# Kernel optimization log

Measured on AMD Instinct MI355X. Metric: run time of the kernel, lower is better.

## Reference

```python
import jax, jax.numpy as jnp
import numpy as np

N, F, D, C, K, E, M = 50000, 512, 128, 128, 3, 20000, 8  # nodes, feat, emb, conv, cheb K, hyperedges, edge size
EPS = 1e-5


def setup_inputs() -> dict:
    key = jax.random.key(0)
    ks = jax.random.split(key, 9)
    pos_set = jax.random.normal(ks[0], (N, F), jnp.float32)
    # each hyperedge = M distinct nodes (contiguous window => distinct, like the original expansion assumes)
    base = jax.random.randint(ks[1], (E, 1), 0, N - M)
    members = (base + jnp.arange(M, dtype=jnp.int32)[None, :]).astype(jnp.int32)  # [E, M]
    # expansion(): full directed clique (no self loops) on the E*M duplicated entries
    row, col = np.where(~np.eye(M, dtype=bool))            # M*(M-1) intra-edge pairs
    offs = np.arange(E, dtype=np.int64)[:, None] * M
    edge_index = jnp.asarray(np.stack([(offs + row[None, :]).ravel(),
                                       (offs + col[None, :]).ravel()]), jnp.int32)  # [2, E*M*(M-1)]
    batch = jnp.asarray(np.repeat(np.arange(E, dtype=np.int64), M), jnp.int32)      # [E*M]
    W_enc = jax.random.normal(ks[2], (F, D), jnp.float32) / np.float32(np.sqrt(F))
    b_enc = jnp.zeros((D,), jnp.float32)
    gn_gamma = 1.0 + 0.1 * jax.random.normal(ks[3], (D,), jnp.float32)
    gn_beta = 0.01 * jax.random.normal(ks[4], (D,), jnp.float32)
    gn_alpha = 1.0 + 0.1 * jax.random.normal(ks[5], (D,), jnp.float32)
    cheb_W = jax.random.normal(ks[6], (K, D, C), jnp.float32) / np.float32(np.sqrt(D * K))
    cheb_b = jnp.zeros((C,), jnp.float32)
    lin_W = jax.random.normal(ks[7], (2 * C, 1), jnp.float32) / np.float32(np.sqrt(2 * C))
    lin_b = jnp.zeros((1,), jnp.float32)
    return dict(pos_set=pos_set, W_enc=W_enc, b_enc=b_enc, gn_gamma=gn_gamma, gn_beta=gn_beta,
                gn_alpha=gn_alpha, cheb_W=cheb_W, cheb_b=cheb_b, lin_W=lin_W, lin_b=lin_b,
                members=members, edge_index=edge_index, batch=batch)


def reference(pos_set, W_enc, b_enc, gn_gamma, gn_beta, gn_alpha, cheb_W, cheb_b,
              lin_W, lin_b, members, edge_index, batch):
    num_entries = E * M
    # running_type == 'structure': Hardtanh(Linear(feature))
    x = jnp.clip(pos_set @ W_enc + b_enc, -1.0, 1.0)                    # [N, D]
    # partition(): duplicate node features per (node, hyperedge) incidence
    xe = x[members.reshape(-1)]                                         # [E*M, D]
    # GraphNorm (per-hyperedge group): out = gamma*(x - alpha*mean)/sqrt(var+eps) + beta
    cnt = jax.ops.segment_sum(jnp.ones((num_entries,), xe.dtype), batch, num_segments=E)  # [E]
    mean = jax.ops.segment_sum(xe, batch, num_segments=E) / cnt[:, None]
    ctr = xe - gn_alpha * mean[batch]
    var = jax.ops.segment_sum(ctr * ctr, batch, num_segments=E) / cnt[:, None]
    xe = gn_gamma * ctr / jnp.sqrt(var + EPS)[batch] + gn_beta
    # AlphaDropout is identity at eval time
    # ChebConv: sym norm, lambda_max=2 => L_hat = -D^{-1/2} A D^{-1/2} (zero diagonal)
    src, dst = edge_index[0], edge_index[1]
    deg = jax.ops.segment_sum(jnp.ones_like(src, dtype=xe.dtype), dst, num_segments=num_entries)
    w = -jax.lax.rsqrt(deg[src] * deg[dst])                             # [nE] scaled-Laplacian weights

    def Lhat(h):  # sparse matvec via gather + segment scatter-add
        return jax.ops.segment_sum(w[:, None] * h[src], dst, num_segments=num_entries)

    Tx0 = xe
    Tx1 = Lhat(Tx0)
    out = Tx0 @ cheb_W[0] + Tx1 @ cheb_W[1]
    Tkm1, Tkm2 = Tx1, Tx0
    for k in range(2, K):  # K is a small static constant
        Tk = 2.0 * Lhat(Tkm1) - Tkm2
        out = out + Tk @ cheb_W[k]
        Tkm1, Tkm2 = Tk, Tkm1
    h = jnp.clip(out + cheb_b, -1.0, 1.0)                               # Hardtanh
    # poolings per hyperedge
    y_max = jax.ops.segment_max(h, batch, num_segments=E)
    y_min = jax.ops.segment_min(h, batch, num_segments=E)
    y_norm = jnp.sqrt(jax.ops.segment_sum(h * h, batch, num_segments=E) / cnt[:, None])
    y = jnp.concatenate([y_max - y_min, y_norm], axis=1)                # [E, 2C]
    logits = y @ lin_W + lin_b
    return jax.nn.sigmoid(logits).squeeze(-1)                           # [E] link probabilities
```

## Files before the change

### kernel.cpp

```cpp
#include <hip/hip_runtime.h>
#include <hip/hip_bf16.h>

#define NN   50000
#define FF   512
#define DD   128
#define CC   128
#define EE   20000
#define MM   8
#define EPSV 1e-5f

typedef __attribute__((ext_vector_type(8)))  short bfrag;
typedef __attribute__((ext_vector_type(4)))  unsigned int u32x4;
typedef __attribute__((ext_vector_type(16))) float f32x16;

__device__ __forceinline__ f32x16 mfma32(u32x4 a, u32x4 b, f32x16 c) {
    return __builtin_amdgcn_mfma_f32_32x32x16_bf16(
        __builtin_bit_cast(bfrag, a), __builtin_bit_cast(bfrag, b), c, 0, 0, 0);
}

__device__ __forceinline__ unsigned short f2bf(float f) {
    unsigned u = __builtin_bit_cast(unsigned, f);
    unsigned r = u + 0x7FFFu + ((u >> 16) & 1u);
    return (unsigned short)(r >> 16);
}
__device__ __forceinline__ float bf2f(unsigned short h) {
    unsigned u = ((unsigned)h) << 16;
    return __builtin_bit_cast(float, u);
}
__device__ __forceinline__ void split1(float a, short& hi, short& lo) {
    unsigned short h = f2bf(a);
    hi = (short)h;
    lo = (short)f2bf(a - bf2f(h));
}

template <int CTRL>
__device__ __forceinline__ float dpp_addstep(float x) {
    const int xi = __builtin_bit_cast(int, x);
    const int yi = __builtin_amdgcn_update_dpp(xi, xi, CTRL, 0xF, 0xF, true);
    return x + __builtin_bit_cast(float, yi);
}
__device__ __forceinline__ float sum8(float x) {
    x = dpp_addstep<0xB1>(x);
    x = dpp_addstep<0x4E>(x);
    x = dpp_addstep<0x141>(x);
    return x;
}

__device__ __forceinline__ void pack_split8(const float* v, u32x4& hi, u32x4& lo) {
#pragma unroll
    for (int p = 0; p < 4; p++) {
        const unsigned u0 = __builtin_bit_cast(unsigned, v[2 * p]);
        const unsigned u1 = __builtin_bit_cast(unsigned, v[2 * p + 1]);
        const unsigned h0 = u0 & 0xFFFF0000u, h1 = u1 & 0xFFFF0000u;
        hi[p] = (u0 >> 16) | h1;
        const float r0 = v[2 * p]     - __builtin_bit_cast(float, h0);
        const float r1 = v[2 * p + 1] - __builtin_bit_cast(float, h1);
        unsigned lp;
        asm("v_cvt_pk_bf16_f32 %0, %1, %2" : "=v"(lp) : "v"(r0), "v"(r1));
        lo[p] = lp;
    }
}
__device__ __forceinline__ void pack8(const float* v, u32x4& w) {
#pragma unroll
    for (int p = 0; p < 4; p++) {
        unsigned lp;
        asm("v_cvt_pk_bf16_f32 %0, %1, %2" : "=v"(lp) : "v"(v[2 * p]), "v"(v[2 * p + 1]));
        w[p] = lp;
    }
}

__global__ void prep_kernel(const float* __restrict__ W_enc,
                            const float* __restrict__ cheb_W,
                            unsigned short* __restrict__ Ep_hi,
                            unsigned short* __restrict__ Ep_lo,
                            unsigned short* __restrict__ Wp_hi,
                            unsigned short* __restrict__ Wp_lo) {
    const int tid = blockIdx.x * blockDim.x + threadIdx.x;
    const int stride = gridDim.x * blockDim.x;
    for (int p = tid; p < 64 * 128; p += stride) {
        const int slot = p >> 7, n = p & 127;
        bfrag fh, fl;
#pragma unroll
        for (int j = 0; j < 8; j++) {
            const float v = W_enc[(size_t)(slot * 8 + j) * DD + n];
            short h, lo; split1(v, h, lo);
            fh[j] = h; fl[j] = lo;
        }
        *(bfrag*)&Ep_hi[(size_t)p * 8] = fh;
        *(bfrag*)&Ep_lo[(size_t)p * 8] = fl;
    }
    const float c1 = 1.0f / 7.0f;
    const float c2 = -47.0f / 49.0f;
    const float c3 = -1.0f / 7.0f;
    const float c4 = 12.0f / 49.0f;
    for (int p = tid; p < 32 * 128; p += stride) {
        const int slot = p >> 7, c = p & 127;
        bfrag fh, fl;
#pragma unroll
        for (int j = 0; j < 8; j++) {
            const int k = slot * 8 + j;
            float v;
            if (k < DD) {
                v = cheb_W[0 * DD * CC + k * CC + c]
                  + c1 * cheb_W[1 * DD * CC + k * CC + c]
                  + c2 * cheb_W[2 * DD * CC + k * CC + c];
            } else {
                const int d = k - DD;
                v = c3 * cheb_W[1 * DD * CC + d * CC + c]
                  + c4 * cheb_W[2 * DD * CC + d * CC + c];
            }
            short h, lo; split1(v, h, lo);
            fh[j] = h; fl[j] = lo;
        }
        *(bfrag*)&Wp_hi[(size_t)p * 8] = fh;
        *(bfrag*)&Wp_lo[(size_t)p * 8] = fl;
    }
}

__global__ __launch_bounds__(128, 4) void enc_kernel(
        const float* __restrict__ pos,
        const unsigned short* __restrict__ Ep_hi,
        const unsigned short* __restrict__ Ep_lo,
        const float* __restrict__ b_enc,
        float* __restrict__ x) {
    const int t = threadIdx.x;
    const int w = t >> 6, l = t & 63, l31 = l & 31, lg2 = l >> 5;

    int arow = blockIdx.x * 32 + l31;
    if (arow >= NN) arow = NN - 1;
    const float* aBase = pos + (size_t)arow * FF + lg2 * 8;

    f32x16 acc[2];
#pragma unroll
    for (int ntl = 0; ntl < 2; ntl++)
#pragma unroll
        for (int i = 0; i < 16; i++) acc[ntl][i] = 0.f;

    auto body = [&](float4 a0, float4 a1, int ks) {
        const float av[8] = {a0.x, a0.y, a0.z, a0.w, a1.x, a1.y, a1.z, a1.w};
        u32x4 ahi, alo;
        pack_split8(av, ahi, alo);
        const int slot = ks * 2 + lg2;
#pragma unroll
        for (int ntl = 0; ntl < 2; ntl++) {
            const int col = w * 64 + ntl * 32 + l31;
            const size_t boff = ((size_t)slot * 128 + col) * 8;
            const u32x4 bhi = *(const u32x4*)(Ep_hi + boff);
            const u32x4 blo = *(const u32x4*)(Ep_lo + boff);
            acc[ntl] = mfma32(ahi, bhi, acc[ntl]);
            acc[ntl] = mfma32(ahi, blo, acc[ntl]);
            acc[ntl] = mfma32(alo, bhi, acc[ntl]);
        }
    };

    float4 pa0 = *(const float4*)(aBase);
    float4 pa1 = *(const float4*)(aBase + 4);
    float4 pb0 = *(const float4*)(aBase + 16);
    float4 pb1 = *(const float4*)(aBase + 20);
    for (int ks = 0; ks < 32; ks += 2) {
        const float4 c0 = pa0, c1 = pa1;
        if (ks + 2 < 32) {
            pa0 = *(const float4*)(aBase + (ks + 2) * 16);
            pa1 = *(const float4*)(aBase + (ks + 2) * 16 + 4);
        }
        body(c0, c1, ks);
        const float4 d0 = pb0, d1 = pb1;
        if (ks + 3 < 32) {
            pb0 = *(const float4*)(aBase + (ks + 3) * 16);
            pb1 = *(const float4*)(aBase + (ks + 3) * 16 + 4);
        }
        body(d0, d1, ks + 1);
    }

    const int brow = blockIdx.x * 32;
#pragma unroll
    for (int ntl = 0; ntl < 2; ntl++) {
        const int col = w * 64 + ntl * 32 + l31;
        const float bias = b_enc[col];
#pragma unroll
        for (int r = 0; r < 16; r++) {
            const int row = brow + (r & 3) + 8 * (r >> 2) + 4 * lg2;
            if (row < NN) {
                const float v = acc[ntl][r] + bias;
                x[(size_t)row * DD + col] = fminf(1.0f, fmaxf(-1.0f, v));
            }
        }
    }
}

__global__ __launch_bounds__(256, 4) void edge_kernel(
        const float* __restrict__ x,
        const int* __restrict__ members,
        const unsigned short* __restrict__ Wp_hi,
        const unsigned short* __restrict__ Wp_lo,
        const float* __restrict__ gn_gamma,
        const float* __restrict__ gn_beta,
        const float* __restrict__ gn_alpha,
        const float* __restrict__ cheb_b,
        const float* __restrict__ lin_W,
        const float* __restrict__ lin_b,
        float* __restrict__ out) {
    const int t = threadIdx.x;
    const int w = t >> 6, l = t & 63, l31 = l & 31, lg2 = l >> 5;

    const int node = members[blockIdx.x * 128 + w * 32 + l31];
    const float* xrow = x + (size_t)node * DD + lg2 * 8;

    f32x16 acc[4];
#pragma unroll
    for (int nt = 0; nt < 4; nt++)
#pragma unroll
        for (int i = 0; i < 16; i++) acc[nt][i] = 0.f;

    auto body = [&](float4 a0, float4 a1, int ks) {
        const int koff = ks * 16 + lg2 * 8;
        const float4 al0 = *(const float4*)(gn_alpha + koff);
        const float4 al1 = *(const float4*)(gn_alpha + koff + 4);
        const float4 g0  = *(const float4*)(gn_gamma + koff);
        const float4 g1  = *(const float4*)(gn_gamma + koff + 4);
        const float4 b0  = *(const float4*)(gn_beta + koff);
        const float4 b1  = *(const float4*)(gn_beta + koff + 4);
        const float al[8] = {al0.x, al0.y, al0.z, al0.w, al1.x, al1.y, al1.z, al1.w};
        const float gm[8] = {g0.x, g0.y, g0.z, g0.w, g1.x, g1.y, g1.z, g1.w};
        const float bt[8] = {b0.x, b0.y, b0.z, b0.w, b1.x, b1.y, b1.z, b1.w};

        const float v[8] = {a0.x, a0.y, a0.z, a0.w, a1.x, a1.y, a1.z, a1.w};
        float s[8], q[8];
#pragma unroll
        for (int j = 0; j < 8; j++) { s[j] = v[j]; q[j] = v[j] * v[j]; }
#pragma unroll
        for (int j = 0; j < 8; j++) s[j] = dpp_addstep<0xB1>(s[j]);
#pragma unroll
        for (int j = 0; j < 8; j++) q[j] = dpp_addstep<0xB1>(q[j]);
#pragma unroll
        for (int j = 0; j < 8; j++) s[j] = dpp_addstep<0x4E>(s[j]);
#pragma unroll
        for (int j = 0; j < 8; j++) q[j] = dpp_addstep<0x4E>(q[j]);
#pragma unroll
        for (int j = 0; j < 8; j++) s[j] = dpp_addstep<0x141>(s[j]);
#pragma unroll
        for (int j = 0; j < 8; j++) q[j] = dpp_addstep<0x141>(q[j]);

        float nv[8], sv[8];
#pragma unroll
        for (int j = 0; j < 8; j++) {
            const float m   = s[j] * 0.125f;
            const float var = q[j] * 0.125f - al[j] * (2.0f - al[j]) * m * m;
            const float sc  = gm[j] * rsqrtf(var + EPSV);
            nv[j] = sc * (v[j] - al[j] * m) + bt[j];
            sv[j] = 8.0f * (sc * m * (1.0f - al[j]) + bt[j]);
        }
        u32x4 ahi, alo, shi;
        pack_split8(nv, ahi, alo);
        pack8(sv, shi);

        const int slotN = ks * 2 + lg2;
        const int slotS = 16 + slotN;
#pragma unroll
        for (int nt = 0; nt < 4; nt++) {
            const int col = nt * 32 + l31;
            const size_t offN = ((size_t)slotN * 128 + col) * 8;
            const size_t offS = ((size_t)slotS * 128 + col) * 8;
            const u32x4 wahi = *(const u32x4*)(Wp_hi + offN);
            const u32x4 walo = *(const u32x4*)(Wp_lo + offN);
            const u32x4 wbh  = *(const u32x4*)(Wp_hi + offS);
            acc[nt] = mfma32(ahi, wahi, acc[nt]);
            acc[nt] = mfma32(ahi, walo, acc[nt]);
            acc[nt] = mfma32(alo, wahi, acc[nt]);
            acc[nt] = mfma32(shi, wbh,  acc[nt]);
        }
    };

    float4 pa0 = *(const float4*)(xrow);
    float4 pa1 = *(const float4*)(xrow + 4);
    float4 pb0 = *(const float4*)(xrow + 16);
    float4 pb1 = *(const float4*)(xrow + 20);
    for (int ks = 0; ks < 8; ks += 2) {
        const float4 c0 = pa0, c1 = pa1;
        if (ks + 2 < 8) {
            pa0 = *(const float4*)(xrow + (ks + 2) * 16);
            pa1 = *(const float4*)(xrow + (ks + 2) * 16 + 4);
        }
        body(c0, c1, ks);
        const float4 d0 = pb0, d1 = pb1;
        if (ks + 3 < 8) {
            pb0 = *(const float4*)(xrow + (ks + 3) * 16);
            pb1 = *(const float4*)(xrow + (ks + 3) * 16 + 4);
        }
        body(d0, d1, ks + 1);
    }

    float p[4] = {0.f, 0.f, 0.f, 0.f};
#pragma unroll
    for (int nt = 0; nt < 4; nt++) {
        const int col = nt * 32 + l31;
        const float bias = cheb_b[col];
        const float w1 = lin_W[col], w2 = lin_W[DD + col];
#pragma unroll
        for (int e = 0; e < 4; e++) {
            float mx = -2.f, mn = 2.f, ssq = 0.f;
#pragma unroll
            for (int q2 = 0; q2 < 4; q2++) {
                float h = acc[nt][e * 4 + q2] + bias;
                h = fminf(1.0f, fmaxf(-1.0f, h));
                mx = fmaxf(mx, h); mn = fminf(mn, h); ssq += h * h;
            }
            mx = fmaxf(mx, __shfl_xor(mx, 32));
            mn = fminf(mn, __shfl_xor(mn, 32));
            ssq += __shfl_xor(ssq, 32);
            p[e] += (mx - mn) * w1 + sqrtf(ssq * 0.125f) * w2;
        }
    }
#pragma unroll
    for (int mk = 1; mk <= 16; mk <<= 1)
#pragma unroll
        for (int e = 0; e < 4; e++) p[e] += __shfl_xor(p[e], mk);
    if (l == 0) {
        const float b0 = lin_b[0];
#pragma unroll
        for (int e = 0; e < 4; e++) {
            const float z = p[e] + b0;
            out[blockIdx.x * 16 + w * 4 + e] = 1.0f / (1.0f + expf(-z));
        }
    }
}

extern "C" void kernel_launch(void* const* d_in, const int* in_sizes, int n_in,
                              void* d_out, int out_size, void* d_ws, size_t ws_size,
                              hipStream_t stream) {
    const float* pos    = (const float*)d_in[0];
    const float* W_enc  = (const float*)d_in[1];
    const float* b_enc  = (const float*)d_in[2];
    const float* gammaP = (const float*)d_in[3];
    const float* betaP  = (const float*)d_in[4];
    const float* alphaP = (const float*)d_in[5];
    const float* cheb_W = (const float*)d_in[6];
    const float* cheb_b = (const float*)d_in[7];
    const float* lin_W  = (const float*)d_in[8];
    const float* lin_b  = (const float*)d_in[9];
    const int*   members = (const int*)d_in[10];
    float* out = (float*)d_out;

    char* ws = (char*)d_ws;
    float* x = (float*)ws;
    unsigned short* Ep_hi = (unsigned short*)(ws + 25600000);
    unsigned short* Ep_lo = Ep_hi + 64 * 128 * 8;
    unsigned short* Wp_hi = Ep_lo + 64 * 128 * 8;
    unsigned short* Wp_lo = Wp_hi + 32 * 128 * 8;

    prep_kernel<<<32, 256, 0, stream>>>(W_enc, cheb_W, Ep_hi, Ep_lo, Wp_hi, Wp_lo);
    enc_kernel<<<(NN + 31) / 32, 128, 0, stream>>>(pos, Ep_hi, Ep_lo, b_enc, x);
    edge_kernel<<<EE / 16, 256, 0, stream>>>(x, members, Wp_hi, Wp_lo,
                                             gammaP, betaP, alphaP, cheb_b, lin_W, lin_b, out);
}
```

Before: 291.0 us.

## Enlarge encoder tile to 64 rows with 4 waves and deepen A prefetch

```diff
diff --git a/kernel.cpp b/kernel.cpp
--- a/kernel.cpp
+++ b/kernel.cpp
@@ -38,12 +38,6 @@
     const int xi = __builtin_bit_cast(int, x);
     const int yi = __builtin_amdgcn_update_dpp(xi, xi, CTRL, 0xF, 0xF, true);
     return x + __builtin_bit_cast(float, yi);
-}
-__device__ __forceinline__ float sum8(float x) {
-    x = dpp_addstep<0xB1>(x);
-    x = dpp_addstep<0x4E>(x);
-    x = dpp_addstep<0x141>(x);
-    return x;
 }
 
 __device__ __forceinline__ void pack_split8(const float* v, u32x4& hi, u32x4& lo) {
@@ -117,7 +111,7 @@
     }
 }
 
-__global__ __launch_bounds__(128, 4) void enc_kernel(
+__global__ __launch_bounds__(256, 4) void enc_kernel(
         const float* __restrict__ pos,
         const unsigned short* __restrict__ Ep_hi,
         const unsigned short* __restrict__ Ep_lo,
@@ -125,8 +119,9 @@
         float* __restrict__ x) {
     const int t = threadIdx.x;
     const int w = t >> 6, l = t & 63, l31 = l & 31, lg2 = l >> 5;
-
-    int arow = blockIdx.x * 32 + l31;
+    const int wm = w & 1, wn = w >> 1;
+
+    int arow = blockIdx.x * 64 + wm * 32 + l31;
     if (arow >= NN) arow = NN - 1;
     const float* aBase = pos + (size_t)arow * FF + lg2 * 8;
 
@@ -143,7 +138,7 @@
         const int slot = ks * 2 + lg2;
 #pragma unroll
         for (int ntl = 0; ntl < 2; ntl++) {
-            const int col = w * 64 + ntl * 32 + l31;
+            const int col = wn * 64 + ntl * 32 + l31;
             const size_t boff = ((size_t)slot * 128 + col) * 8;
             const u32x4 bhi = *(const u32x4*)(Ep_hi + boff);
             const u32x4 blo = *(const u32x4*)(Ep_lo + boff);
@@ -153,29 +148,34 @@
         }
     };
 
-    float4 pa0 = *(const float4*)(aBase);
-    float4 pa1 = *(const float4*)(aBase + 4);
-    float4 pb0 = *(const float4*)(aBase + 16);
-    float4 pb1 = *(const float4*)(aBase + 20);
-    for (int ks = 0; ks < 32; ks += 2) {
-        const float4 c0 = pa0, c1 = pa1;
-        if (ks + 2 < 32) {
-            pa0 = *(const float4*)(aBase + (ks + 2) * 16);
-            pa1 = *(const float4*)(aBase + (ks + 2) * 16 + 4);
-        }
+    float4 q0a = *(const float4*)(aBase +  0), q0b = *(const float4*)(aBase +  4);
+    float4 q1a = *(const float4*)(aBase + 16), q1b = *(const float4*)(aBase + 20);
+    float4 q2a = *(const float4*)(aBase + 32), q2b = *(const float4*)(aBase + 36);
+    float4 q3a = *(const float4*)(aBase + 48), q3b = *(const float4*)(aBase + 52);
+    for (int ks = 0; ks < 32; ks += 4) {
+        float4 c0, c1;
+        c0 = q0a; c1 = q0b;
+        if (ks + 4 < 32) { q0a = *(const float4*)(aBase + (ks + 4) * 16);
+                           q0b = *(const float4*)(aBase + (ks + 4) * 16 + 4); }
         body(c0, c1, ks);
-        const float4 d0 = pb0, d1 = pb1;
-        if (ks + 3 < 32) {
-            pb0 = *(const float4*)(aBase + (ks + 3) * 16);
-            pb1 = *(const float4*)(aBase + (ks + 3) * 16 + 4);
-        }
-        body(d0, d1, ks + 1);
-    }
-
-    const int brow = blockIdx.x * 32;
+        c0 = q1a; c1 = q1b;
+        if (ks + 5 < 32) { q1a = *(const float4*)(aBase + (ks + 5) * 16);
+                           q1b = *(const float4*)(aBase + (ks + 5) * 16 + 4); }
+        body(c0, c1, ks + 1);
+        c0 = q2a; c1 = q2b;
+        if (ks + 6 < 32) { q2a = *(const float4*)(aBase + (ks + 6) * 16);
+                           q2b = *(const float4*)(aBase + (ks + 6) * 16 + 4); }
+        body(c0, c1, ks + 2);
+        c0 = q3a; c1 = q3b;
+        if (ks + 7 < 32) { q3a = *(const float4*)(aBase + (ks + 7) * 16);
+                           q3b = *(const float4*)(aBase + (ks + 7) * 16 + 4); }
+        body(c0, c1, ks + 3);
+    }
+
+    const int brow = blockIdx.x * 64 + wm * 32;
 #pragma unroll
     for (int ntl = 0; ntl < 2; ntl++) {
-        const int col = w * 64 + ntl * 32 + l31;
+        const int col = wn * 64 + ntl * 32 + l31;
         const float bias = b_enc[col];
 #pragma unroll
         for (int r = 0; r < 16; r++) {
@@ -188,7 +188,7 @@
     }
 }
 
-__global__ __launch_bounds__(256, 4) void edge_kernel(
+__global__ __launch_bounds__(256, 3) void edge_kernel(
         const float* __restrict__ x,
         const int* __restrict__ members,
         const unsigned short* __restrict__ Wp_hi,
@@ -349,7 +349,7 @@
     unsigned short* Wp_lo = Wp_hi + 32 * 128 * 8;
 
     prep_kernel<<<32, 256, 0, stream>>>(W_enc, cheb_W, Ep_hi, Ep_lo, Wp_hi, Wp_lo);
-    enc_kernel<<<(NN + 31) / 32, 128, 0, stream>>>(pos, Ep_hi, Ep_lo, b_enc, x);
+    enc_kernel<<<(NN + 63) / 64, 256, 0, stream>>>(pos, Ep_hi, Ep_lo, b_enc, x);
     edge_kernel<<<EE / 16, 256, 0, stream>>>(x, members, Wp_hi, Wp_lo,
                                              gammaP, betaP, alphaP, cheb_b, lin_W, lin_b, out);
 }
```

After: 264.6 us. -9.1%, faster.
